# Optimization experiments

Measured on AMD Instinct MI355X. Metric: run time of the kernel, lower is better.

## Reference

```python
import jax, jax.numpy as jnp
import numpy as np

NH = 8      # num_heads
DK = 160    # total key/query depth
DV = 64     # total value depth
DKH = DK // NH  # 20
DVH = DV // NH  # 8


def conv2d(x, w, b, pad):
    y = jax.lax.conv_general_dilated(
        x, w, window_strides=(1, 1), padding=[(pad, pad), (pad, pad)],
        dimension_numbers=('NCHW', 'OIHW', 'NCHW'))
    return y + b[None, :, None, None]


def rel_to_abs(x):
    # x: (B, Hd, L, 2L-1) -> (B, Hd, L, L)
    B, Hd, L, _ = x.shape
    x = jnp.pad(x, ((0, 0), (0, 0), (0, 0), (0, 1)))          # (B,Hd,L,2L)
    flat = x.reshape(B, Hd, L * 2 * L)
    flat = jnp.pad(flat, ((0, 0), (0, 0), (0, L - 1)))
    final = flat.reshape(B, Hd, L + 1, 2 * L - 1)
    return final[:, :, :L, L - 1:]


def relative_logits_1d(q, rel_k, H, W, perm):
    # q: (B, NH, H, W, DKH); NOTE: einsum output drops head axis -> sums over heads,
    # exactly as in the torch source ('bhxyd,md->bxym').
    rl = jnp.einsum('bhxyd,md->bxym', q, rel_k)               # (B,H,W,2W-1)
    rl = rel_to_abs(rl.reshape(-1, H, W, 2 * W - 1))          # (B,H,W,W)
    B = rl.shape[0]
    rl = rl[:, None, :, None, :, :]                           # (B,1,H,1,W,W)
    rl = jnp.broadcast_to(rl, (B, NH, H, H, W, W))
    rl = jnp.transpose(rl, perm)
    return rl.reshape(B, NH, H * W, H * W)


def setup_inputs() -> dict:
    key = jax.random.key(0)
    ks = jax.random.split(key, 9)
    s = 0.05
    return {
        'x': jax.random.normal(ks[0], (8, 256, 32, 32), jnp.float32),
        'kqv_w': jax.random.normal(ks[1], (384, 256, 1, 1), jnp.float32) * s,
        'kqv_b': jax.random.normal(ks[2], (384,), jnp.float32) * s,
        'conv_out_w': jax.random.normal(ks[3], (192, 256, 3, 3), jnp.float32) * s,
        'conv_out_b': jax.random.normal(ks[4], (192,), jnp.float32) * s,
        'attn_w': jax.random.normal(ks[5], (64, 64, 1, 1), jnp.float32) * s,
        'attn_b': jax.random.normal(ks[6], (64,), jnp.float32) * s,
        'rel_h': jax.random.normal(ks[7], (63, 20), jnp.float32),
        'rel_w': jax.random.normal(ks[8], (63, 20), jnp.float32),
    }


def reference(x, kqv_w, kqv_b, conv_out_w, conv_out_b, attn_w, attn_b, rel_h, rel_w):
    B, C, H, W = x.shape
    kqv = conv2d(x, kqv_w, kqv_b, 0)
    k, q, v = kqv[:, :DK], kqv[:, DK:2 * DK], kqv[:, 2 * DK:]
    q = q * (DKH ** -0.5)
    # split_heads_2d in the source is a raw reshape (no transpose); replicate exactly
    k = k.reshape(B, NH, H, W, DKH)
    q = q.reshape(B, NH, H, W, DKH)
    v = v.reshape(B, NH, H, W, DVH)
    qf = q.reshape(B, NH, H * W, DKH)
    kf = k.reshape(B, NH, H * W, DKH)
    vf = v.reshape(B, NH, H * W, DVH)
    qk = jnp.einsum('bnid,bnjd->bnij', qf, kf)                # (B,NH,HW,HW)
    qr_w_l = relative_logits_1d(q, rel_w, H, W, (0, 1, 2, 4, 3, 5))
    qr_h_l = relative_logits_1d(jnp.swapaxes(q, 2, 3), rel_h, W, H, (0, 1, 4, 2, 5, 3))
    weights = jax.nn.softmax(qk + qr_h_l + qr_w_l, axis=-1)
    attn = jnp.matmul(weights, vf)                            # (B,NH,HW,DVH)
    attn = attn.reshape(B, NH, DVH, H, W).reshape(B, DV, H, W)  # raw reshapes as in source
    attn = conv2d(attn, attn_w, attn_b, 0)
    return jnp.concatenate([conv2d(x, conv_out_w, conv_out_b, 1), attn], axis=1)
```

## Files before the change

### kernel.cpp

```cpp
#include <hip/hip_runtime.h>

constexpr float QSCALE = 0.22360679774997896f;
constexpr float LOG2E  = 1.4426950408889634f;

typedef __attribute__((ext_vector_type(8))) short bf16x8;
typedef __attribute__((ext_vector_type(4))) float f32x4;

__device__ __forceinline__ unsigned short f2bf(float f) {
    unsigned u = __float_as_uint(f);
    u = (u + 0x7FFFu + ((u >> 16) & 1u)) >> 16;
    return (unsigned short)u;
}

__device__ __forceinline__ unsigned cvt_pk_bf16(float lo, float hi) {
    unsigned r;
    asm("v_cvt_pk_bf16_f32 %0, %1, %2" : "=v"(r) : "v"(lo), "v"(hi));
    return r;
}

__device__ __forceinline__ void qk_decomp(unsigned flat, int& n, int& i, int& d) {
    n = flat / 20480u;
    unsigned r = flat - (unsigned)n * 20480u;
    i = r / 20u;
    d = r - (unsigned)i * 20u;
}

__global__ __launch_bounds__(256) void pack_inputs_kernel(
    const float* __restrict__ X, const float* __restrict__ Wconv,
    const float* __restrict__ Wkqv, const float* __restrict__ Wattn,
    unsigned short* __restrict__ Xt2, unsigned short* __restrict__ Xq,
    unsigned short* __restrict__ Wp, unsigned short* __restrict__ Wq,
    unsigned short* __restrict__ Kb, unsigned short* __restrict__ Qb,
    unsigned short* __restrict__ VtF, unsigned short* __restrict__ Wa)
{
    int t = blockIdx.x * 256 + threadIdx.x;
    if (t < 295936) {
        int b = t / 36992, rem = t - b * 36992;
        int chunk = rem / 4624; int rem2 = rem - chunk * 4624;
        int kc = rem2 / 1156;   int spad = rem2 - kc * 1156;
        int yp = spad / 34, xp = spad - yp * 34;
        bf16x8 v = {};
        if (yp >= 1 && yp <= 32 && xp >= 1 && xp <= 32) {
            const float* src = X + (size_t)b * 262144
                                 + (size_t)(chunk * 32 + kc * 8) * 1024
                                 + (yp - 1) * 32 + (xp - 1);
            #pragma unroll
            for (int j = 0; j < 8; ++j) v[j] = (short)f2bf(src[(size_t)j * 1024]);
        }
        *(bf16x8*)&Xt2[(((size_t)b * 8 + chunk) * 1156 + spad) * 32 + kc * 8] = v;
    } else if (t < 558080) {
        int t2 = t - 295936;
        int lane = t2 & 63;
        int chunk = (t2 >> 6) & 7;
        int g16 = (t2 >> 9) & 63;
        int b = t2 >> 15;
        int sp = g16 * 16 + (lane & 15);
        const float* src = X + (size_t)b * 262144
                             + (size_t)(chunk * 32 + (lane >> 4) * 8) * 1024 + sp;
        bf16x8 v;
        #pragma unroll
        for (int j = 0; j < 8; ++j) v[j] = (short)f2bf(src[(size_t)j * 1024]);
        *(bf16x8*)&Xq[(size_t)t2 * 8] = v;
    } else if (t < 613376) {
        int t2 = t - 558080;
        int l = t2 & 63;
        int rb = (t2 >> 6) & 3;
        int ks = (t2 >> 8) % 72;
        int ot = t2 / 18432;
        int oc = ot * 64 + rb * 16 + (l & 15);
        int kbase = ks * 32 + (l >> 4) * 8;
        bf16x8 v;
        #pragma unroll
        for (int j = 0; j < 8; ++j) {
            int kp = kbase + j;
            int r = kp >> 8, c = kp & 255;
            v[j] = (short)f2bf(Wconv[((size_t)oc * 256 + c) * 9 + r]);
        }
        *(bf16x8*)&Wp[(size_t)t2 * 8] = v;
    } else if (t < 625664) {
        int t2 = t - 613376;
        int l = t2 & 63;
        int rb = (t2 >> 6) & 3;
        int ks = (t2 >> 8) & 7;
        int ot = t2 / 2048;
        int oc = ot * 64 + rb * 16 + (l & 15);
        float sc = (oc >= 160 && oc < 320) ? QSCALE : 1.0f;
        int kbase = ks * 32 + (l >> 4) * 8;
        bf16x8 v;
        #pragma unroll
        for (int j = 0; j < 8; ++j)
            v[j] = (short)f2bf(Wkqv[(size_t)oc * 256 + kbase + j] * sc);
        *(bf16x8*)&Wq[(size_t)t2 * 8] = v;
    } else if (t < 691200) {
        int row = t - 625664;
        bf16x8 z = {};
        *(uint2*)&Kb[(size_t)row * 32 + 20] = make_uint2(0u, 0u);
        *(bf16x8*)&Kb[(size_t)row * 32 + 24] = z;
    } else if (t < 756736) {
        int row = t - 691200;
        bf16x8 z = {};
        *(uint2*)&Qb[(size_t)row * 32 + 20] = make_uint2(0u, 0u);
        *(bf16x8*)&Qb[(size_t)row * 32 + 24] = z;
    } else if (t < 822272) {
        int t2 = t - 756736;
        int bn = t2 >> 10;
        int G = (t2 >> 5) & 31;
        int r8 = (t2 >> 2) & 7;
        int ksub = t2 & 3;
        unsigned short fill = (r8 == 0) ? 0x3F80 : 0;
        bf16x8 v = {short(fill), short(fill), short(fill), short(fill),
                    short(fill), short(fill), short(fill), short(fill)};
        *(bf16x8*)&VtF[(((size_t)bn * 32 + G) * 64 + (8 + r8) + ksub * 16) * 8] = v;
    } else {
        int t2 = t - 822272;
        int l = t2 & 63;
        int rb = (t2 >> 6) & 3;
        int kchunk = t2 >> 8;
        int oc = rb * 16 + (l & 15);
        int kbase = kchunk * 32 + (l >> 4) * 8;
        bf16x8 v;
        #pragma unroll
        for (int j = 0; j < 8; ++j)
            v[j] = (short)f2bf(Wattn[(size_t)oc * 64 + kbase + j]);
        *(bf16x8*)&Wa[(size_t)t2 * 8] = v;
    }
}

__global__ __launch_bounds__(512) void mfma_gemms_kernel(
    const unsigned short* __restrict__ Wp, const unsigned short* __restrict__ Wq,
    const unsigned short* __restrict__ Xt2, const unsigned short* __restrict__ Xq,
    const float* __restrict__ cbias, const float* __restrict__ qbias,
    float* __restrict__ out, float* __restrict__ qf32,
    unsigned short* __restrict__ Kb, unsigned short* __restrict__ Qb,
    unsigned short* __restrict__ VtF)
{
    const int b  = blockIdx.z;
    const int ty = blockIdx.y;
    const int s0 = blockIdx.x * 64;
    const int tid = threadIdx.x;
    const int lane = tid & 63, w = tid >> 6;
    const int kc = lane >> 4, ln = lane & 15;

    __shared__ float comb[4][64][17];

    f32x4 acc00 = {}, acc01 = {}, acc10 = {}, acc11 = {};

    if (ty < 3) {
        const int kh = w >> 2, wr = (w >> 1) & 1, wc = w & 1;
        const int wq = wr * 2 + wc;
        const int Y = blockIdx.x * 2;
        const size_t aoff0 = ((size_t)(ty * 288 + wr * 2) * 64 + lane) * 8;
        const size_t aoff1 = aoff0 + 512;
        const int spad0 = (Y + wc + 1) * 34 + 1 + ln;
        const unsigned short* xb = Xt2 + (size_t)b * 8 * 36992;

        #pragma unroll 1
        for (int cc2 = 0; cc2 < 4; ++cc2) {
            const int cc = kh * 4 + cc2;
            bf16x8 A0[9], A1[9];
            #pragma unroll
            for (int r = 0; r < 9; ++r) {
                A0[r] = *(const bf16x8*)&Wp[aoff0 + (size_t)(r * 8 + cc) * 2048];
                A1[r] = *(const bf16x8*)&Wp[aoff1 + (size_t)(r * 8 + cc) * 2048];
            }
            const unsigned short* xc = xb + (size_t)cc * 36992 + kc * 8;
            #pragma unroll
            for (int r = 0; r < 9; ++r) {
                const int off = (r / 3 - 1) * 34 + (r % 3 - 1);
                const unsigned short* bp = xc + (size_t)(spad0 + off) * 32;
                bf16x8 b0 = *(const bf16x8*)bp;
                bf16x8 b1 = *(const bf16x8*)(bp + 512);
                acc00 = __builtin_amdgcn_mfma_f32_16x16x32_bf16(A0[r], b0, acc00, 0, 0, 0);
                acc01 = __builtin_amdgcn_mfma_f32_16x16x32_bf16(A0[r], b1, acc01, 0, 0, 0);
                acc10 = __builtin_amdgcn_mfma_f32_16x16x32_bf16(A1[r], b0, acc10, 0, 0, 0);
                acc11 = __builtin_amdgcn_mfma_f32_16x16x32_bf16(A1[r], b1, acc11, 0, 0, 0);
            }
        }

        if (kh == 1) {
            float* c0 = &comb[wq][lane][0];
            #pragma unroll
            for (int r = 0; r < 4; ++r) {
                c0[r]      = acc00[r];
                c0[4 + r]  = acc01[r];
                c0[8 + r]  = acc10[r];
                c0[12 + r] = acc11[r];
            }
        }
        __syncthreads();
        if (kh == 0) {
            const float* c0 = &comb[wq][lane][0];
            #pragma unroll
            for (int r = 0; r < 4; ++r) {
                acc00[r] += c0[r];
                acc01[r] += c0[4 + r];
                acc10[r] += c0[8 + r];
                acc11[r] += c0[12 + r];
            }
            const int ocb = ty * 64 + wr * 32;
            const int scol = s0 + wc * 32 + ln;
            float* ob = out + (size_t)b * 262144;
            #pragma unroll
            for (int r = 0; r < 4; ++r) {
                int oc0 = ocb + kc * 4 + r;
                float b0v = cbias[oc0];
                ob[(size_t)oc0 * 1024 + scol]      = acc00[r] + b0v;
                ob[(size_t)oc0 * 1024 + scol + 16] = acc01[r] + b0v;
                int oc1 = oc0 + 16;
                float b1v = cbias[oc1];
                ob[(size_t)oc1 * 1024 + scol]      = acc10[r] + b1v;
                ob[(size_t)oc1 * 1024 + scol + 16] = acc11[r] + b1v;
            }
        }
    } else {
        const int ot = ty - 3;
        const int wr = w >> 2, wc = w & 3;
        const size_t aoff0 = ((size_t)(ot * 32 + wr * 2) * 64 + lane) * 8;
        const size_t aoff1 = aoff0 + 512;
        const int g0 = blockIdx.x * 4 + wc;
        const size_t xb0 = (((size_t)b * 64 + g0) * 8) * 512 + lane * 8;

        #pragma unroll
        for (int cc = 0; cc < 8; ++cc) {
            bf16x8 a0 = *(const bf16x8*)&Wq[aoff0 + (size_t)cc * 2048];
            bf16x8 a1 = *(const bf16x8*)&Wq[aoff1 + (size_t)cc * 2048];
            bf16x8 b0 = *(const bf16x8*)&Xq[xb0 + (size_t)cc * 512];
            acc00 = __builtin_amdgcn_mfma_f32_16x16x32_bf16(a0, b0, acc00, 0, 0, 0);
            acc10 = __builtin_amdgcn_mfma_f32_16x16x32_bf16(a1, b0, acc10, 0, 0, 0);
        }

        const int ocb = ot * 64 + wr * 32;
        const int scol = s0 + wc * 16 + ln;
        const int b8 = b * 8;
        #pragma unroll
        for (int r = 0; r < 4; ++r) {
            #pragma unroll
            for (int e = 0; e < 2; ++e) {
                int oc  = ocb + e * 16 + kc * 4 + r;
                float val = e ? acc10[r] : acc00[r];
                int col = scol;
                if (oc < 160) {
                    float v = val + qbias[oc];
                    int n, i, d; qk_decomp((unsigned)oc * 1024u + col, n, i, d);
                    Kb[(((size_t)(b8 + n) * 1024 + i) << 5) + d] = f2bf(v);
                } else if (oc < 320) {
                    float v = val + qbias[oc] * QSCALE;
                    unsigned flat = (unsigned)(oc - 160) * 1024u + col;
                    qf32[(size_t)b * 163840 + flat] = v;
                    int n, i, d; qk_decomp(flat, n, i, d);
                    Qb[(((size_t)(b8 + n) * 1024 + i) << 5) + d] = f2bf(v * LOG2E);
                } else {
                    float v = val + qbias[oc];
                    unsigned flat = (unsigned)(oc - 320) * 1024u + col;
                    int n = flat >> 13, i = (flat >> 3) & 1023, dd = flat & 7;
                    int G = i >> 5, k0 = i & 31;
                    VtF[((((size_t)(b8 + n) * 32 + G) * 64) + dd + ((k0 >> 3) << 4)) * 8
                        + (k0 & 7)] = f2bf(v);
                }
            }
        }
    }
}

__global__ __launch_bounds__(256) void rel_kernel(
    const float* __restrict__ qf32,
    const float* __restrict__ rel_h, const float* __restrict__ rel_w,
    float* __restrict__ Rh, float* __restrict__ Rw)
{
    const int blk = blockIdx.x;
    const int b = blk >> 6, st = blk & 63;
    const int s0 = st * 16;
    const int tid = threadIdx.x;
    __shared__ float rhS[63][21];
    __shared__ float rwS[63][21];
    __shared__ float qs[16][20];

    for (int i = tid; i < 1260; i += 256) {
        int mm = i / 20, d = i - mm * 20;
        rhS[mm][d] = rel_h[i];
        rwS[mm][d] = rel_w[i];
    }
    for (int e = tid; e < 320; e += 256) {
        int s = e / 20, d = e - s * 20;
        const float* qb = qf32 + (size_t)b * 163840 + (s0 + s) * 20 + d;
        float acc = 0.0f;
        #pragma unroll
        for (int n = 0; n < 8; ++n) acc += qb[(size_t)n * 20480];
        qs[s][d] = acc;
    }
    __syncthreads();

    for (int p = tid; p < 1008; p += 256) {
        int s = p / 63, mm = p - s * 63;
        float sh = 0.0f, sw = 0.0f;
        #pragma unroll
        for (int d = 0; d < 20; ++d) {
            float qv = qs[s][d];
            sh += qv * rhS[mm][d];
            sw += qv * rwS[mm][d];
        }
        int sg = s0 + s;
        int y = sg >> 5, x = sg & 31;
        Rw[(size_t)b * 64512 + sg * 63 + mm] = sw * LOG2E;
        Rh[(size_t)b * 64512 + (x * 32 + y) * 63 + mm] = sh * LOG2E;
    }
}

__global__ __launch_bounds__(256, 4) void attn_mfma_kernel(
    const unsigned short* __restrict__ Qb, const unsigned short* __restrict__ Kb,
    const unsigned short* __restrict__ VtF, const float* __restrict__ Rh,
    const float* __restrict__ Rw, float* __restrict__ attnout)
{
    const int bn = blockIdx.y;
    const int b = bn >> 3;
    const int i0 = blockIdx.x * 64;
    const int tid = threadIdx.x;
    const int lane = tid & 63, w = tid >> 6;

    __shared__ float RhS[64][33];
    __shared__ float RwS[64][33];
    __shared__ unsigned short Pl[4][16][72];
    {
        int q = tid & 63, seg = tid >> 6;
        int i = i0 + q, y1 = i >> 5, x1 = i & 31;
        const float* rh = Rh + (size_t)b * 64512 + (x1 * 32 + y1) * 63 + 31 - y1 + seg * 8;
        const float* rw = Rw + (size_t)b * 64512 + i * 63 + 31 - x1 + seg * 8;
        #pragma unroll
        for (int j = 0; j < 8; ++j) {
            RhS[q][seg * 8 + j] = rh[j];
            RwS[q][seg * 8 + j] = rw[j];
        }
    }
    __syncthreads();

    const int ql = lane & 15, g = lane >> 4;
    const int qw = i0 + w * 16;

    bf16x8 qf = *(const bf16x8*)&Qb[((size_t)bn * 1024 + qw + ql) * 32 + g * 8];
    const unsigned short* kp = Kb + ((size_t)bn * 1024 + ql) * 32 + g * 8;
    const unsigned short* vp = VtF + (size_t)bn * 32 * 512 + lane * 8;

    const float* rhrow = &RhS[w * 16 + ql][0];
    float rwA[4], rwB[4];
    #pragma unroll
    for (int r = 0; r < 4; ++r) {
        rwA[r] = RwS[w * 16 + ql][4 * g + r];
        rwB[r] = RwS[w * 16 + ql][16 + 4 * g + r];
    }

    f32x4 oaccT = {};

    bf16x8 c0 = *(const bf16x8*)&kp[0 * 512];
    bf16x8 c1 = *(const bf16x8*)&kp[1 * 512];
    bf16x8 c2 = *(const bf16x8*)&kp[2 * 512];
    bf16x8 c3 = *(const bf16x8*)&kp[3 * 512];

    #pragma unroll 2
    for (int kt = 0; kt < 16; ++kt) {
        __builtin_amdgcn_s_setprio(1);
        f32x4 s0 = {}, s1 = {}, s2 = {}, s3 = {};
        s0 = __builtin_amdgcn_mfma_f32_16x16x32_bf16(c0, qf, s0, 0, 0, 0);
        s1 = __builtin_amdgcn_mfma_f32_16x16x32_bf16(c1, qf, s1, 0, 0, 0);
        s2 = __builtin_amdgcn_mfma_f32_16x16x32_bf16(c2, qf, s2, 0, 0, 0);
        s3 = __builtin_amdgcn_mfma_f32_16x16x32_bf16(c3, qf, s3, 0, 0, 0);
        __builtin_amdgcn_s_setprio(0);

        if (kt < 15) {
            kp += 2048;
            c0 = *(const bf16x8*)&kp[0 * 512];
            c1 = *(const bf16x8*)&kp[1 * 512];
            c2 = *(const bf16x8*)&kp[2 * 512];
            c3 = *(const bf16x8*)&kp[3 * 512];
        }

        float rh0 = rhrow[2 * kt];
        float rh1 = rhrow[2 * kt + 1];

        float p00 = exp2f(s0[0] + rh0 + rwA[0]), p01 = exp2f(s0[1] + rh0 + rwA[1]);
        float p02 = exp2f(s0[2] + rh0 + rwA[2]), p03 = exp2f(s0[3] + rh0 + rwA[3]);
        float p10 = exp2f(s1[0] + rh0 + rwB[0]), p11 = exp2f(s1[1] + rh0 + rwB[1]);
        float p12 = exp2f(s1[2] + rh0 + rwB[2]), p13 = exp2f(s1[3] + rh0 + rwB[3]);
        float p20 = exp2f(s2[0] + rh1 + rwA[0]), p21 = exp2f(s2[1] + rh1 + rwA[1]);
        float p22 = exp2f(s2[2] + rh1 + rwA[2]), p23 = exp2f(s2[3] + rh1 + rwA[3]);
        float p30 = exp2f(s3[0] + rh1 + rwB[0]), p31 = exp2f(s3[1] + rh1 + rwB[1]);
        float p32 = exp2f(s3[2] + rh1 + rwB[2]), p33 = exp2f(s3[3] + rh1 + rwB[3]);

        const int key = 4 * g;
        *(unsigned*)&Pl[w][ql][key]      = cvt_pk_bf16(p00, p01);
        *(unsigned*)&Pl[w][ql][key + 2]  = cvt_pk_bf16(p02, p03);
        *(unsigned*)&Pl[w][ql][key + 16] = cvt_pk_bf16(p10, p11);
        *(unsigned*)&Pl[w][ql][key + 18] = cvt_pk_bf16(p12, p13);
        *(unsigned*)&Pl[w][ql][key + 32] = cvt_pk_bf16(p20, p21);
        *(unsigned*)&Pl[w][ql][key + 34] = cvt_pk_bf16(p22, p23);
        *(unsigned*)&Pl[w][ql][key + 48] = cvt_pk_bf16(p30, p31);
        *(unsigned*)&Pl[w][ql][key + 50] = cvt_pk_bf16(p32, p33);

        #pragma unroll
        for (int half = 0; half < 2; ++half) {
            bf16x8 vfr = *(const bf16x8*)&vp[(size_t)(kt * 2 + half) * 512];
            bf16x8 pfr = *(const bf16x8*)&Pl[w][ql][half * 32 + g * 8];
            __builtin_amdgcn_s_setprio(1);
            oaccT = __builtin_amdgcn_mfma_f32_16x16x32_bf16(vfr, pfr, oaccT, 0, 0, 0);
            __builtin_amdgcn_s_setprio(0);
        }
    }

    float lsum = __shfl(oaccT[0], 32 + ql, 64);
    float inv = 1.0f / lsum;
    if (g < 2) {
        float4 o = {oaccT[0] * inv, oaccT[1] * inv, oaccT[2] * inv, oaccT[3] * inv};
        *(float4*)&attnout[((size_t)bn * 1024 + qw + ql) * 8 + g * 4] = o;
    }
}

__global__ __launch_bounds__(256) void attn_out_mfma_kernel(
    const unsigned short* __restrict__ Wa, const float* __restrict__ attn,
    const float* __restrict__ bias, float* __restrict__ out)
{
    const int b = blockIdx.y;
    const int tid = threadIdx.x;
    const int w = tid >> 6, lane = tid & 63;
    const int sg = blockIdx.x * 4 + w;
    const int kc = lane >> 4, ln = lane & 15;
    const int s = sg * 16 + ln;

    const float* ab = attn + (size_t)b * 65536 + s;

    f32x4 acc0 = {}, acc1 = {}, acc2 = {}, acc3 = {};
    #pragma unroll
    for (int kchunk = 0; kchunk < 2; ++kchunk) {
        const int c0 = kchunk * 32 + kc * 8;
        const float* cp = ab + (size_t)c0 * 1024;
        bf16x8 bf;
        #pragma unroll
        for (int j = 0; j < 8; j += 2) {
            unsigned u = cvt_pk_bf16(cp[(size_t)j * 1024], cp[(size_t)(j + 1) * 1024]);
            bf[j]     = (short)u;
            bf[j + 1] = (short)(u >> 16);
        }

        const unsigned short* wp = Wa + (size_t)kchunk * 2048;
        bf16x8 a0 = *(const bf16x8*)&wp[(size_t)(0 * 64 + lane) * 8];
        bf16x8 a1 = *(const bf16x8*)&wp[(size_t)(1 * 64 + lane) * 8];
        bf16x8 a2 = *(const bf16x8*)&wp[(size_t)(2 * 64 + lane) * 8];
        bf16x8 a3 = *(const bf16x8*)&wp[(size_t)(3 * 64 + lane) * 8];
        acc0 = __builtin_amdgcn_mfma_f32_16x16x32_bf16(a0, bf, acc0, 0, 0, 0);
        acc1 = __builtin_amdgcn_mfma_f32_16x16x32_bf16(a1, bf, acc1, 0, 0, 0);
        acc2 = __builtin_amdgcn_mfma_f32_16x16x32_bf16(a2, bf, acc2, 0, 0, 0);
        acc3 = __builtin_amdgcn_mfma_f32_16x16x32_bf16(a3, bf, acc3, 0, 0, 0);
    }

    float* ob = out + ((size_t)b * 256 + 192) * 1024 + s;
    #pragma unroll
    for (int r = 0; r < 4; ++r) {
        int oc0 = 0 * 16 + kc * 4 + r;
        int oc1 = 1 * 16 + kc * 4 + r;
        int oc2 = 2 * 16 + kc * 4 + r;
        int oc3 = 3 * 16 + kc * 4 + r;
        ob[(size_t)oc0 * 1024] = acc0[r] + bias[oc0];
        ob[(size_t)oc1 * 1024] = acc1[r] + bias[oc1];
        ob[(size_t)oc2 * 1024] = acc2[r] + bias[oc2];
        ob[(size_t)oc3 * 1024] = acc3[r] + bias[oc3];
    }
}

extern "C" void kernel_launch(void* const* d_in, const int* in_sizes, int n_in,
                              void* d_out, int out_size, void* d_ws, size_t ws_size,
                              hipStream_t stream)
{
    const float* x          = (const float*)d_in[0];
    const float* kqv_w      = (const float*)d_in[1];
    const float* kqv_b      = (const float*)d_in[2];
    const float* conv_out_w = (const float*)d_in[3];
    const float* conv_out_b = (const float*)d_in[4];
    const float* attn_w     = (const float*)d_in[5];
    const float* attn_b     = (const float*)d_in[6];
    const float* rel_h      = (const float*)d_in[7];
    const float* rel_w      = (const float*)d_in[8];
    float* out = (float*)d_out;
    float* ws  = (float*)d_ws;

    float* ws_qf32 = ws;
    float* ws_rw   = ws + 1310720;
    float* ws_rh   = ws + 1826816;
    float* ws_attn = ws + 2342912;
    unsigned short* Qb  = (unsigned short*)(ws + 2867200);
    unsigned short* Kb  = (unsigned short*)(ws + 3915776);
    unsigned short* VtF = (unsigned short*)(ws + 4964352);
    unsigned short* Xt2 = (unsigned short*)(ws + 5488640);
    unsigned short* Xq  = (unsigned short*)(ws + 6672384);
    unsigned short* Wp  = (unsigned short*)(ws + 7720960);
    unsigned short* Wq  = (unsigned short*)(ws + 7942144);
    unsigned short* Wa  = (unsigned short*)(ws + 7991296);

    pack_inputs_kernel<<<3214, 256, 0, stream>>>(
        x, conv_out_w, kqv_w, attn_w, Xt2, Xq, Wp, Wq, Kb, Qb, VtF, Wa);
    mfma_gemms_kernel<<<dim3(16, 9, 8), 512, 0, stream>>>(
        Wp, Wq, Xt2, Xq, conv_out_b, kqv_b, out, ws_qf32, Kb, Qb, VtF);
    rel_kernel<<<512, 256, 0, stream>>>(ws_qf32, rel_h, rel_w, ws_rh, ws_rw);
    attn_mfma_kernel<<<dim3(16, 64), 256, 0, stream>>>(
        Qb, Kb, VtF, ws_rh, ws_rw, ws_attn);
    attn_out_mfma_kernel<<<dim3(16, 8), 256, 0, stream>>>(
        Wa, ws_attn, attn_b, out);
}
```

Measured before the change: 94.88 us.

## Drop split-K in conv GEMM and widen per-wave tiles in 256-thread blocks

The 3x3 conv GEMM previously split the channel reduction across two wave groups and combined the partial sums through shared memory behind a barrier. Now each of 4 waves runs the full 8-chunk reduction, which removes the LDS combine and the __syncthreads. The kqv GEMM branch now has each wave compute a 2x2 tile instead of 2x1, so it reuses each weight fragment across two B fragments. Blocks shrink to 256 threads, which halves the waves per block and lengthens each wave's serial reduction, so latency hiding may suffer.

```diff
diff --git a/kernel.cpp b/kernel.cpp
--- a/kernel.cpp
+++ b/kernel.cpp
@@ -126,7 +126,7 @@
     }
 }
 
-__global__ __launch_bounds__(512) void mfma_gemms_kernel(
+__global__ __launch_bounds__(256) void mfma_gemms_kernel(
     const unsigned short* __restrict__ Wp, const unsigned short* __restrict__ Wq,
     const unsigned short* __restrict__ Xt2, const unsigned short* __restrict__ Xq,
     const float* __restrict__ cbias, const float* __restrict__ qbias,
@@ -139,15 +139,13 @@
     const int s0 = blockIdx.x * 64;
     const int tid = threadIdx.x;
     const int lane = tid & 63, w = tid >> 6;
+    const int wr = w >> 1, wc = w & 1;
     const int kc = lane >> 4, ln = lane & 15;
 
-    __shared__ float comb[4][64][17];
-
     f32x4 acc00 = {}, acc01 = {}, acc10 = {}, acc11 = {};
+    const int scol = s0 + wc * 32 + ln;
 
     if (ty < 3) {
-        const int kh = w >> 2, wr = (w >> 1) & 1, wc = w & 1;
-        const int wq = wr * 2 + wc;
         const int Y = blockIdx.x * 2;
         const size_t aoff0 = ((size_t)(ty * 288 + wr * 2) * 64 + lane) * 8;
         const size_t aoff1 = aoff0 + 512;
@@ -155,8 +153,7 @@
         const unsigned short* xb = Xt2 + (size_t)b * 8 * 36992;
 
         #pragma unroll 1
-        for (int cc2 = 0; cc2 < 4; ++cc2) {
-            const int cc = kh * 4 + cc2;
+        for (int cc = 0; cc < 8; ++cc) {
             bf16x8 A0[9], A1[9];
             #pragma unroll
             for (int r = 0; r < 9; ++r) {
@@ -177,68 +174,49 @@
             }
         }
 
-        if (kh == 1) {
-            float* c0 = &comb[wq][lane][0];
-            #pragma unroll
-            for (int r = 0; r < 4; ++r) {
-                c0[r]      = acc00[r];
-                c0[4 + r]  = acc01[r];
-                c0[8 + r]  = acc10[r];
-                c0[12 + r] = acc11[r];
-            }
-        }
-        __syncthreads();
-        if (kh == 0) {
-            const float* c0 = &comb[wq][lane][0];
-            #pragma unroll
-            for (int r = 0; r < 4; ++r) {
-                acc00[r] += c0[r];
-                acc01[r] += c0[4 + r];
-                acc10[r] += c0[8 + r];
-                acc11[r] += c0[12 + r];
-            }
-            const int ocb = ty * 64 + wr * 32;
-            const int scol = s0 + wc * 32 + ln;
-            float* ob = out + (size_t)b * 262144;
-            #pragma unroll
-            for (int r = 0; r < 4; ++r) {
-                int oc0 = ocb + kc * 4 + r;
-                float b0v = cbias[oc0];
-                ob[(size_t)oc0 * 1024 + scol]      = acc00[r] + b0v;
-                ob[(size_t)oc0 * 1024 + scol + 16] = acc01[r] + b0v;
-                int oc1 = oc0 + 16;
-                float b1v = cbias[oc1];
-                ob[(size_t)oc1 * 1024 + scol]      = acc10[r] + b1v;
-                ob[(size_t)oc1 * 1024 + scol + 16] = acc11[r] + b1v;
-            }
+        const int ocb = ty * 64 + wr * 32;
+        float* ob = out + (size_t)b * 262144;
+        #pragma unroll
+        for (int r = 0; r < 4; ++r) {
+            int oc0 = ocb + kc * 4 + r;
+            float b0v = cbias[oc0];
+            ob[(size_t)oc0 * 1024 + scol]      = acc00[r] + b0v;
+            ob[(size_t)oc0 * 1024 + scol + 16] = acc01[r] + b0v;
+            int oc1 = oc0 + 16;
+            float b1v = cbias[oc1];
+            ob[(size_t)oc1 * 1024 + scol]      = acc10[r] + b1v;
+            ob[(size_t)oc1 * 1024 + scol + 16] = acc11[r] + b1v;
         }
     } else {
         const int ot = ty - 3;
-        const int wr = w >> 2, wc = w & 3;
         const size_t aoff0 = ((size_t)(ot * 32 + wr * 2) * 64 + lane) * 8;
         const size_t aoff1 = aoff0 + 512;
-        const int g0 = blockIdx.x * 4 + wc;
+        const int g0 = blockIdx.x * 4 + wc * 2;
         const size_t xb0 = (((size_t)b * 64 + g0) * 8) * 512 + lane * 8;
+        const size_t xb1 = xb0 + 4096;
 
         #pragma unroll
         for (int cc = 0; cc < 8; ++cc) {
             bf16x8 a0 = *(const bf16x8*)&Wq[aoff0 + (size_t)cc * 2048];
             bf16x8 a1 = *(const bf16x8*)&Wq[aoff1 + (size_t)cc * 2048];
             bf16x8 b0 = *(const bf16x8*)&Xq[xb0 + (size_t)cc * 512];
+            bf16x8 b1 = *(const bf16x8*)&Xq[xb1 + (size_t)cc * 512];
             acc00 = __builtin_amdgcn_mfma_f32_16x16x32_bf16(a0, b0, acc00, 0, 0, 0);
+            acc01 = __builtin_amdgcn_mfma_f32_16x16x32_bf16(a0, b1, acc01, 0, 0, 0);
             acc10 = __builtin_amdgcn_mfma_f32_16x16x32_bf16(a1, b0, acc10, 0, 0, 0);
+            acc11 = __builtin_amdgcn_mfma_f32_16x16x32_bf16(a1, b1, acc11, 0, 0, 0);
         }
 
         const int ocb = ot * 64 + wr * 32;
-        const int scol = s0 + wc * 16 + ln;
         const int b8 = b * 8;
         #pragma unroll
         for (int r = 0; r < 4; ++r) {
             #pragma unroll
-            for (int e = 0; e < 2; ++e) {
-                int oc  = ocb + e * 16 + kc * 4 + r;
-                float val = e ? acc10[r] : acc00[r];
-                int col = scol;
+            for (int e = 0; e < 4; ++e) {
+                int oc  = ocb + (e >> 1) * 16 + kc * 4 + r;
+                int col = scol + (e & 1) * 16;
+                float val = (e == 0) ? acc00[r] : (e == 1) ? acc01[r]
+                          : (e == 2) ? acc10[r] : acc11[r];
                 if (oc < 160) {
                     float v = val + qbias[oc];
                     int n, i, d; qk_decomp((unsigned)oc * 1024u + col, n, i, d);
@@ -495,7 +473,7 @@
 
     pack_inputs_kernel<<<3214, 256, 0, stream>>>(
         x, conv_out_w, kqv_w, attn_w, Xt2, Xq, Wp, Wq, Kb, Qb, VtF, Wa);
-    mfma_gemms_kernel<<<dim3(16, 9, 8), 512, 0, stream>>>(
+    mfma_gemms_kernel<<<dim3(16, 9, 8), 256, 0, stream>>>(
         Wp, Wq, Xt2, Xq, conv_out_b, kqv_b, out, ws_qf32, Kb, Qb, VtF);
     rel_kernel<<<512, 256, 0, stream>>>(ws_qf32, rel_h, rel_w, ws_rh, ws_rw);
     attn_mfma_kernel<<<dim3(16, 64), 256, 0, stream>>>(
```

After: 83.75 us, median of 2. -11.7%, faster.
